# Optimization experiments

Hardware: AMD Instinct MI355X
Metric: run time of the kernel (lower is better)

The kernel has to match this reference:

```python
import jax, jax.numpy as jnp
import numpy as np

_MIN_BLOCK_KV = 32


def setup_inputs() -> dict:
    key = jax.random.key(0)
    k0, k1, k2, k3 = jax.random.split(key, 4)
    B, H, HKV, D, T, S = 32, 32, 8, 128, 2048, 8
    pool = B * T
    q = jax.random.normal(k0, (B, H, D), dtype=jnp.float32)
    k_buffer = jax.random.normal(k1, (pool, HKV, D), dtype=jnp.float32)
    v_buffer = jax.random.normal(k2, (pool, HKV, D), dtype=jnp.float32)
    # uniform contexts: request b owns tokens [b*T, (b+1)*T) of the pool, in permuted (paged) order
    kv_indptr = (jnp.arange(B + 1, dtype=jnp.int32) * T)
    kv_indices = jax.random.permutation(k3, pool).astype(jnp.int32)
    num_kv_splits = jnp.full((B,), S, dtype=jnp.int32)
    return {"q": q, "k_buffer": k_buffer, "v_buffer": v_buffer,
            "kv_indptr": kv_indptr, "kv_indices": kv_indices,
            "num_kv_splits": num_kv_splits}


def reference(q, k_buffer, v_buffer, kv_indptr, kv_indices, num_kv_splits):
    # Paged KV-cache decode attention, stage 1 (split-KV partial softmax).
    B, H, D = q.shape
    HKV = k_buffer.shape[1]
    Lv = v_buffer.shape[-1]
    G = H // HKV                       # GQA group size
    sm_scale = 1.0 / (D ** 0.5)        # Model default (sm_scale=None)
    logit_cap = 0.0                    # Model default -> capping disabled

    seq_lens = kv_indptr[1:] - kv_indptr[:-1]          # [B]
    T = kv_indices.shape[0] // B                       # max context len (uniform setup)
    S = int(jnp.max(num_kv_splits))                    # max_kv_splits (eager, as in torch code)

    pos = jnp.arange(T, dtype=jnp.int32)               # [T]
    valid = pos[None, :] < seq_lens[:, None]           # [B,T]
    # gather KV pool locations per (batch, position); clamp OOB positions
    gidx = kv_indptr[:-1, None] + jnp.minimum(pos[None, :], seq_lens[:, None] - 1)
    kv_loc = kv_indices[gidx]                          # [B,T]
    k_g = k_buffer[kv_loc]                             # [B,T,HKV,D]
    v_g = v_buffer[kv_loc]                             # [B,T,HKV,Lv]

    qr = q.reshape(B, HKV, G, D)
    qk = jnp.einsum('bkgd,btkd->bkgt', qr, k_g) * sm_scale   # [B,HKV,G,T]
    if logit_cap > 0:
        qk = logit_cap * jnp.tanh(qk / logit_cap)

    # split assignment: kv_len_per_split = cdiv(cdiv(seq_len, splits), MIN) * MIN
    cdiv = lambda a, b: (a + b - 1) // b
    kv_len_per_split = cdiv(cdiv(seq_lens, num_kv_splits), _MIN_BLOCK_KV) * _MIN_BLOCK_KV  # [B]
    split_id = pos[None, :] // kv_len_per_split[:, None]      # [B,T]
    split_mask = (split_id[:, None, :] == jnp.arange(S, dtype=jnp.int32)[None, :, None]) \
                 & valid[:, None, :]                          # [B,S,T]

    neg_inf = jnp.float32(-jnp.inf)
    masked = jnp.where(split_mask[:, None, None, :, :], qk[:, :, :, None, :], neg_inf)  # [B,HKV,G,S,T]
    m = jnp.max(masked, axis=-1)                               # [B,HKV,G,S]
    m_safe = jnp.where(jnp.isfinite(m), m, 0.0)                # guard empty splits
    p = jnp.exp(masked - m_safe[..., None])                    # [B,HKV,G,S,T]
    p = jnp.where(split_mask[:, None, None, :, :], p, 0.0)
    e_sum = jnp.sum(p, axis=-1)                                # [B,HKV,G,S]
    acc = jnp.einsum('bkgst,btkv->bkgsv', p, v_g)              # [B,HKV,G,S,Lv]

    att_out = (acc / e_sum[..., None]).reshape(B, H, S, Lv)
    att_lse = (m + jnp.log(e_sum)).reshape(B, H, S)
    return att_out, att_lse
```

## Files before the change

kernel.cpp:

```cpp
#include <hip/hip_runtime.h>
#include <math.h>


namespace {
constexpr int kB = 32;
constexpr int kH = 32;
constexpr int kHKV = 8;
constexpr int kD = 128;
constexpr int kG = kH / kHKV;
constexpr int kS = 8;
constexpr int kMinBlockKV = 32;
constexpr int kDepth = 3;
}

__device__ __forceinline__ void gload16(const float* g, float* l) {
    __builtin_amdgcn_global_load_lds(
        (const __attribute__((address_space(1))) void*)g,
        (__attribute__((address_space(3))) void*)l,
        16, 0, 0);
}

__global__ __launch_bounds__(256, 2) void decode_split_kernel(
    const float* __restrict__ q,
    const float* __restrict__ k_buffer,
    const float* __restrict__ v_buffer,
    const int* __restrict__ kv_indptr,
    const int* __restrict__ kv_indices,
    const int* __restrict__ num_kv_splits,
    float* __restrict__ att_out,
    float* __restrict__ att_lse)
{
    const int bid = blockIdx.x;
    const int s  = bid % kS;
    const int kh = (bid / kS) % kHKV;
    const int b  = bid / (kS * kHKV);

    const int tid  = threadIdx.x;
    const int wave = tid >> 6;
    const int lane = tid & 63;
    const int tg   = lane >> 4;
    const int li   = lane & 15;

    const int ptr0    = kv_indptr[b];
    const int seq_len = kv_indptr[b + 1] - ptr0;
    const int splits  = num_kv_splits[b];
    const int per     = (seq_len + splits - 1) / splits;
    const int lps     = ((per + kMinBlockKV - 1) / kMinBlockKV) * kMinBlockKV;
    const int t0 = s * lps;
    const int t1 = min(t0 + lps, seq_len);

    const float sm_scale = 0.08838834764831845f;

    __shared__ float stage[4][kDepth][2][512];

    float4 q0[kG], q1[kG];
    const float* qb = q + ((size_t)b * kH + (size_t)kh * kG) * kD;
    #pragma unroll
    for (int g = 0; g < kG; ++g) {
        float4 a = *(const float4*)(qb + (size_t)g * kD + li * 4);
        float4 c = *(const float4*)(qb + (size_t)g * kD + 64 + li * 4);
        q0[g] = make_float4(a.x * sm_scale, a.y * sm_scale, a.z * sm_scale, a.w * sm_scale);
        q1[g] = make_float4(c.x * sm_scale, c.y * sm_scale, c.z * sm_scale, c.w * sm_scale);
    }

    float  l[kG] = {0.f, 0.f, 0.f, 0.f};
    float4 a0[kG], a1[kG];
    #pragma unroll
    for (int g = 0; g < kG; ++g) {
        a0[g] = make_float4(0.f, 0.f, 0.f, 0.f);
        a1[g] = make_float4(0.f, 0.f, 0.f, 0.f);
    }

    for (int base = t0 + wave * 64; base < t1; base += 256) {
        const int nt = min(64, t1 - base);
        int my_loc = 0;
        if (lane < nt) my_loc = kv_indices[ptr0 + base + lane];
        const int ng = (nt + 3) >> 2;

#define ISSUE(IG)                                                            \
        {                                                                    \
            const int _ig   = (IG);                                          \
            const int _slot = _ig % kDepth;                                  \
            const int _pair = lane >> 5;                                     \
            const int _o32  = (lane & 31) * 4;                               \
            const int _iA = min(_ig * 4 + _pair,     nt - 1);                \
            const int _iB = min(_ig * 4 + 2 + _pair, nt - 1);                \
            const int _lA = __shfl(my_loc, _iA);                             \
            const int _lB = __shfl(my_loc, _iB);                             \
            const size_t _rA = ((size_t)_lA * kHKV + kh) * kD;               \
            const size_t _rB = ((size_t)_lB * kHKV + kh) * kD;               \
            gload16(k_buffer + _rA + _o32, &stage[wave][_slot][0][0]);       \
            gload16(k_buffer + _rB + _o32, &stage[wave][_slot][0][256]);     \
            gload16(v_buffer + _rA + _o32, &stage[wave][_slot][1][0]);       \
            gload16(v_buffer + _rB + _o32, &stage[wave][_slot][1][256]);     \
        }

        if (ng > 0) ISSUE(0)
        if (ng > 1) ISSUE(1)
        if (ng > 2) ISSUE(2)

        for (int ig = 0; ig < ng; ++ig) {
            const int slot = ig % kDepth;
            const int rem  = ng - 1 - ig;
            if (rem >= 2)      asm volatile("s_waitcnt vmcnt(8)" ::: "memory");
            else if (rem == 1) asm volatile("s_waitcnt vmcnt(4)" ::: "memory");
            else               asm volatile("s_waitcnt vmcnt(0)" ::: "memory");
            __builtin_amdgcn_sched_barrier(0);

            const float* kp = &stage[wave][slot][0][tg * 128];
            const float* vp = &stage[wave][slot][1][tg * 128];
            float4 ck0 = *(const float4*)(kp + li * 4);
            float4 ck1 = *(const float4*)(kp + 64 + li * 4);
            float4 cv0 = *(const float4*)(vp + li * 4);
            float4 cv1 = *(const float4*)(vp + 64 + li * 4);

            asm volatile("s_waitcnt lgkmcnt(0)" ::: "memory");
            __builtin_amdgcn_sched_barrier(0);

            if (ig + kDepth < ng) ISSUE(ig + kDepth)

            float dot[kG];
            #pragma unroll
            for (int g = 0; g < kG; ++g) {
                float d = q0[g].x * ck0.x;
                d = fmaf(q0[g].y, ck0.y, d);
                d = fmaf(q0[g].z, ck0.z, d);
                d = fmaf(q0[g].w, ck0.w, d);
                d = fmaf(q1[g].x, ck1.x, d);
                d = fmaf(q1[g].y, ck1.y, d);
                d = fmaf(q1[g].z, ck1.z, d);
                d = fmaf(q1[g].w, ck1.w, d);
                dot[g] = d;
            }
            #pragma unroll
            for (int m = 1; m <= 8; m <<= 1) {
                #pragma unroll
                for (int g = 0; g < kG; ++g)
                    dot[g] += __shfl_xor(dot[g], m);
            }

            const bool valid = (ig * 4 + tg) < nt;
            #pragma unroll
            for (int g = 0; g < kG; ++g) {
                const float p = valid ? __expf(dot[g]) : 0.f;
                l[g] += p;
                a0[g].x = fmaf(p, cv0.x, a0[g].x);
                a0[g].y = fmaf(p, cv0.y, a0[g].y);
                a0[g].z = fmaf(p, cv0.z, a0[g].z);
                a0[g].w = fmaf(p, cv0.w, a0[g].w);
                a1[g].x = fmaf(p, cv1.x, a1[g].x);
                a1[g].y = fmaf(p, cv1.y, a1[g].y);
                a1[g].z = fmaf(p, cv1.z, a1[g].z);
                a1[g].w = fmaf(p, cv1.w, a1[g].w);
            }
        }
#undef ISSUE
    }

    #pragma unroll
    for (int m = 16; m <= 32; m <<= 1) {
        #pragma unroll
        for (int g = 0; g < kG; ++g) {
            a0[g].x += __shfl_xor(a0[g].x, m);
            a0[g].y += __shfl_xor(a0[g].y, m);
            a0[g].z += __shfl_xor(a0[g].z, m);
            a0[g].w += __shfl_xor(a0[g].w, m);
            a1[g].x += __shfl_xor(a1[g].x, m);
            a1[g].y += __shfl_xor(a1[g].y, m);
            a1[g].z += __shfl_xor(a1[g].z, m);
            a1[g].w += __shfl_xor(a1[g].w, m);
            l[g] += __shfl_xor(l[g], m);
        }
    }

    __syncthreads();
    float* s_acc = &stage[0][0][0][0];
    float* s_l   = s_acc + 4 * kG * kD;
    if (tg == 0) {
        #pragma unroll
        for (int g = 0; g < kG; ++g) {
            *(float4*)&s_acc[(wave * kG + g) * kD + li * 4]      = a0[g];
            *(float4*)&s_acc[(wave * kG + g) * kD + 64 + li * 4] = a1[g];
        }
        if (li == 0) {
            #pragma unroll
            for (int g = 0; g < kG; ++g) s_l[wave * kG + g] = l[g];
        }
    }
    __syncthreads();

    const int g = tid >> 6;
    const int d = (tid & 63) * 2;
    float o0 = 0.f, o1 = 0.f, ls = 0.f;
    #pragma unroll
    for (int w = 0; w < 4; ++w) {
        o0 += s_acc[(w * kG + g) * kD + d];
        o1 += s_acc[(w * kG + g) * kD + d + 1];
        ls += s_l[w * kG + g];
    }
    const float inv = 1.0f / ls;
    const size_t hidx = (size_t)b * kH + (size_t)kh * kG + g;
    float* outp = att_out + (hidx * kS + s) * kD + d;
    outp[0] = o0 * inv;
    outp[1] = o1 * inv;
    if ((tid & 63) == 0)
        att_lse[hidx * kS + s] = logf(ls);
}

extern "C" void kernel_launch(void* const* d_in, const int* in_sizes, int n_in,
                              void* d_out, int out_size, void* d_ws, size_t ws_size,
                              hipStream_t stream) {
    const float* q             = (const float*)d_in[0];
    const float* k_buffer      = (const float*)d_in[1];
    const float* v_buffer      = (const float*)d_in[2];
    const int*   kv_indptr     = (const int*)d_in[3];
    const int*   kv_indices    = (const int*)d_in[4];
    const int*   num_kv_splits = (const int*)d_in[5];

    float* att_out = (float*)d_out;
    float* att_lse = att_out + (size_t)kB * kH * kS * kD;

    dim3 grid(kB * kHKV * kS);
    decode_split_kernel<<<grid, 256, 0, stream>>>(
        q, k_buffer, v_buffer, kv_indptr, kv_indices, num_kv_splits,
        att_out, att_lse);
}
```

Before: 533.3 us.

## Load four KV heads per token contiguously with 512-thread blocks

Restructures the kernel so each block covers four adjacent KV heads for one batch and split. Each wave fetches whole 2KB contiguous rows, four heads per token for K and V, into double-buffered LDS tiles of 8 tokens, instead of per-head 512B segments. The goal is better memory coalescing and fewer, larger gathers from the paged pool. In exchange it adds block-wide barriers every tile, only two-deep prefetching, and a grid four times smaller (512 blocks of 512 threads), which may reduce latency hiding.

```diff
diff --git a/kernel.cpp b/kernel.cpp
--- a/kernel.cpp
+++ b/kernel.cpp
@@ -10,7 +10,9 @@
 constexpr int kG = kH / kHKV;
 constexpr int kS = 8;
 constexpr int kMinBlockKV = 32;
-constexpr int kDepth = 3;
+constexpr int kHB = 4;
+constexpr int kTT = 8;
+constexpr int kChunk = 512;
 }
 
 __device__ __forceinline__ void gload16(const float* g, float* l) {
@@ -20,7 +22,7 @@
         16, 0, 0);
 }
 
-__global__ __launch_bounds__(256, 2) void decode_split_kernel(
+__global__ __launch_bounds__(512, 2) void decode_split_kernel(
     const float* __restrict__ q,
     const float* __restrict__ k_buffer,
     const float* __restrict__ v_buffer,
@@ -31,15 +33,18 @@
     float* __restrict__ att_lse)
 {
     const int bid = blockIdx.x;
-    const int s  = bid % kS;
-    const int kh = (bid / kS) % kHKV;
-    const int b  = bid / (kS * kHKV);
+    const int hh  = bid & 1;
+    const int s   = (bid >> 1) & (kS - 1);
+    const int b   = bid >> 4;
+    const int kh0 = hh * kHB;
 
     const int tid  = threadIdx.x;
     const int wave = tid >> 6;
     const int lane = tid & 63;
     const int tg   = lane >> 4;
     const int li   = lane & 15;
+    const int hkv_l = wave >> 1;
+    const int sub   = wave & 1;
 
     const int ptr0    = kv_indptr[b];
     const int seq_len = kv_indptr[b + 1] - ptr0;
@@ -51,10 +56,10 @@
 
     const float sm_scale = 0.08838834764831845f;
 
-    __shared__ float stage[4][kDepth][2][512];
+    __shared__ float stage[2][kTT][2][kHB * kD];
 
     float4 q0[kG], q1[kG];
-    const float* qb = q + ((size_t)b * kH + (size_t)kh * kG) * kD;
+    const float* qb = q + ((size_t)b * kH + (size_t)(kh0 + hkv_l) * kG) * kD;
     #pragma unroll
     for (int g = 0; g < kG; ++g) {
         float4 a = *(const float4*)(qb + (size_t)g * kD + li * 4);
@@ -71,44 +76,37 @@
         a1[g] = make_float4(0.f, 0.f, 0.f, 0.f);
     }
 
-    for (int base = t0 + wave * 64; base < t1; base += 256) {
-        const int nt = min(64, t1 - base);
-        int my_loc = 0;
-        if (lane < nt) my_loc = kv_indices[ptr0 + base + lane];
-        const int ng = (nt + 3) >> 2;
-
-#define ISSUE(IG)                                                            \
+    for (int chunk = t0; chunk < t1; chunk += kChunk) {
+        const int nt    = min(kChunk, t1 - chunk);
+        const int ntile = (nt + kTT - 1) / kTT;
+
+        int my_loc = kv_indices[ptr0 + min(chunk + lane * kTT + wave, t1 - 1)];
+        asm volatile("s_waitcnt vmcnt(0) lgkmcnt(0)" ::: "memory");
+
+#define ISSUE(T)                                                             \
         {                                                                    \
-            const int _ig   = (IG);                                          \
-            const int _slot = _ig % kDepth;                                  \
-            const int _pair = lane >> 5;                                     \
-            const int _o32  = (lane & 31) * 4;                               \
-            const int _iA = min(_ig * 4 + _pair,     nt - 1);                \
-            const int _iB = min(_ig * 4 + 2 + _pair, nt - 1);                \
-            const int _lA = __shfl(my_loc, _iA);                             \
-            const int _lB = __shfl(my_loc, _iB);                             \
-            const size_t _rA = ((size_t)_lA * kHKV + kh) * kD;               \
-            const size_t _rB = ((size_t)_lB * kHKV + kh) * kD;               \
-            gload16(k_buffer + _rA + _o32, &stage[wave][_slot][0][0]);       \
-            gload16(k_buffer + _rB + _o32, &stage[wave][_slot][0][256]);     \
-            gload16(v_buffer + _rA + _o32, &stage[wave][_slot][1][0]);       \
-            gload16(v_buffer + _rB + _o32, &stage[wave][_slot][1][256]);     \
-        }
-
-        if (ng > 0) ISSUE(0)
-        if (ng > 1) ISSUE(1)
-        if (ng > 2) ISSUE(2)
-
-        for (int ig = 0; ig < ng; ++ig) {
-            const int slot = ig % kDepth;
-            const int rem  = ng - 1 - ig;
-            if (rem >= 2)      asm volatile("s_waitcnt vmcnt(8)" ::: "memory");
-            else if (rem == 1) asm volatile("s_waitcnt vmcnt(4)" ::: "memory");
-            else               asm volatile("s_waitcnt vmcnt(0)" ::: "memory");
+            const int _loc = __shfl(my_loc, (T));                            \
+            float* _dk = &stage[(T) & 1][wave][0][0];                        \
+            float* _dv = &stage[(T) & 1][wave][1][0];                        \
+            const float* _kb = k_buffer + ((size_t)_loc * kHKV + kh0) * kD + lane * 4; \
+            const float* _vb = v_buffer + ((size_t)_loc * kHKV + kh0) * kD + lane * 4; \
+            gload16(_kb,       _dk);                                         \
+            gload16(_kb + 256, _dk + 256);                                   \
+            gload16(_vb,       _dv);                                         \
+            gload16(_vb + 256, _dv + 256);                                   \
+        }
+
+        if (ntile > 0) ISSUE(0)
+        if (ntile > 1) ISSUE(1)
+
+        for (int t = 0; t < ntile; ++t) {
+            if (t + 1 < ntile) { asm volatile("s_waitcnt vmcnt(4)" ::: "memory"); }
+            else               { asm volatile("s_waitcnt vmcnt(0)" ::: "memory"); }
+            __builtin_amdgcn_s_barrier();
             __builtin_amdgcn_sched_barrier(0);
 
-            const float* kp = &stage[wave][slot][0][tg * 128];
-            const float* vp = &stage[wave][slot][1][tg * 128];
+            const float* kp = &stage[t & 1][sub * 4 + tg][0][hkv_l * kD];
+            const float* vp = &stage[t & 1][sub * 4 + tg][1][hkv_l * kD];
             float4 ck0 = *(const float4*)(kp + li * 4);
             float4 ck1 = *(const float4*)(kp + 64 + li * 4);
             float4 cv0 = *(const float4*)(vp + li * 4);
@@ -116,8 +114,9 @@
 
             asm volatile("s_waitcnt lgkmcnt(0)" ::: "memory");
             __builtin_amdgcn_sched_barrier(0);
-
-            if (ig + kDepth < ng) ISSUE(ig + kDepth)
+            __builtin_amdgcn_s_barrier();
+
+            if (t + 2 < ntile) ISSUE(t + 2)
 
             float dot[kG];
             #pragma unroll
@@ -139,7 +138,7 @@
                     dot[g] += __shfl_xor(dot[g], m);
             }
 
-            const bool valid = (ig * 4 + tg) < nt;
+            const bool valid = (t * kTT + sub * 4 + tg) < nt;
             #pragma unroll
             for (int g = 0; g < kG; ++g) {
                 const float p = valid ? __expf(dot[g]) : 0.f;
@@ -174,36 +173,39 @@
     }
 
     __syncthreads();
-    float* s_acc = &stage[0][0][0][0];
-    float* s_l   = s_acc + 4 * kG * kD;
+    float* comb  = &stage[0][0][0][0];
+    float* combl = comb + 4096;
     if (tg == 0) {
+        const int base = (hkv_l * 2 + sub) * kG;
         #pragma unroll
         for (int g = 0; g < kG; ++g) {
-            *(float4*)&s_acc[(wave * kG + g) * kD + li * 4]      = a0[g];
-            *(float4*)&s_acc[(wave * kG + g) * kD + 64 + li * 4] = a1[g];
+            *(float4*)&comb[(base + g) * kD + li * 4]      = a0[g];
+            *(float4*)&comb[(base + g) * kD + 64 + li * 4] = a1[g];
         }
         if (li == 0) {
             #pragma unroll
-            for (int g = 0; g < kG; ++g) s_l[wave * kG + g] = l[g];
+            for (int g = 0; g < kG; ++g) combl[base + g] = l[g];
         }
     }
     __syncthreads();
 
-    const int g = tid >> 6;
-    const int d = (tid & 63) * 2;
-    float o0 = 0.f, o1 = 0.f, ls = 0.f;
-    #pragma unroll
-    for (int w = 0; w < 4; ++w) {
-        o0 += s_acc[(w * kG + g) * kD + d];
-        o1 += s_acc[(w * kG + g) * kD + d + 1];
-        ls += s_l[w * kG + g];
-    }
+    const int ohkv = tid >> 7;
+    const int og   = (tid >> 5) & 3;
+    const int od   = (tid & 31) * 4;
+    const int i0 = (ohkv * 2 + 0) * kG + og;
+    const int i1 = (ohkv * 2 + 1) * kG + og;
+    float4 x0 = *(float4*)&comb[i0 * kD + od];
+    float4 x1 = *(float4*)&comb[i1 * kD + od];
+    const float ls  = combl[i0] + combl[i1];
     const float inv = 1.0f / ls;
-    const size_t hidx = (size_t)b * kH + (size_t)kh * kG + g;
-    float* outp = att_out + (hidx * kS + s) * kD + d;
-    outp[0] = o0 * inv;
-    outp[1] = o1 * inv;
-    if ((tid & 63) == 0)
+    float4 o;
+    o.x = (x0.x + x1.x) * inv;
+    o.y = (x0.y + x1.y) * inv;
+    o.z = (x0.z + x1.z) * inv;
+    o.w = (x0.w + x1.w) * inv;
+    const size_t hidx = (size_t)b * kH + (size_t)(kh0 + ohkv) * kG + og;
+    *(float4*)(att_out + (hidx * kS + s) * kD + od) = o;
+    if (od == 0)
         att_lse[hidx * kS + s] = logf(ls);
 }
 
@@ -220,8 +222,8 @@
     float* att_out = (float*)d_out;
     float* att_lse = att_out + (size_t)kB * kH * kS * kD;
 
-    dim3 grid(kB * kHKV * kS);
-    decode_split_kernel<<<grid, 256, 0, stream>>>(
+    dim3 grid(kB * kS * 2);
+    decode_split_kernel<<<grid, 512, 0, stream>>>(
         q, k_buffer, v_buffer, kv_indptr, kv_indices, num_kv_splits,
         att_out, att_lse);
 }
```

After: 527.0 us. About the same (-1.2%).
